# Kernel tuning notes

Measured on AMD Instinct MI355X. Metric: run time of the kernel, lower is better.

The kernel has to match this reference:

```python
import jax, jax.numpy as jnp
import numpy as np

B, N, D, NE, NB = 512, 128, 64, 6, 4

def setup_inputs() -> dict:
    key = jax.random.key(0)
    ks = jax.random.split(key, 24)
    inp = {}
    inp['atom_types'] = jax.random.randint(ks[0], (B, N), 0, NE, dtype=jnp.int32)
    inp['positions'] = jax.random.normal(ks[1], (B, N, 3), dtype=jnp.float32)
    inp['bonds'] = jax.random.randint(ks[2], (B, N, N), 0, 5, dtype=jnp.int32)
    s = 0.05
    inp['emb'] = jax.random.normal(ks[3], (NE, D), dtype=jnp.float32)
    inp['ae_w'] = jax.random.normal(ks[4], (D,), dtype=jnp.float32) * s
    inp['ae_b'] = jax.random.normal(ks[5], (), dtype=jnp.float32) * s
    inp['ent_w'] = jax.random.normal(ks[6], (D,), dtype=jnp.float32) * s
    inp['ent_b'] = jax.random.normal(ks[7], (), dtype=jnp.float32) * s
    inp['bW'] = jax.random.normal(ks[8], (NB, D, D), dtype=jnp.float32) * s
    inp['bb'] = jax.random.normal(ks[9], (NB,), dtype=jnp.float32) * s
    H = N * D
    inp['sW1'] = jax.random.normal(ks[10], (H, 256), dtype=jnp.float32) * s
    inp['sb1'] = jnp.zeros((256,), jnp.float32)
    inp['sW2'] = jax.random.normal(ks[11], (256, 128), dtype=jnp.float32) * s
    inp['sb2'] = jnp.zeros((128,), jnp.float32)
    inp['sW3'] = jax.random.normal(ks[12], (128, 1), dtype=jnp.float32) * s
    inp['sb3'] = jnp.zeros((1,), jnp.float32)
    inp['dW1'] = jax.random.normal(ks[13], (H, 256), dtype=jnp.float32) * s
    inp['db1'] = jnp.zeros((256,), jnp.float32)
    inp['dW2'] = jax.random.normal(ks[14], (256, 128), dtype=jnp.float32) * s
    inp['db2'] = jnp.zeros((128,), jnp.float32)
    inp['dW3'] = jax.random.normal(ks[15], (128, 1), dtype=jnp.float32) * s
    inp['db3'] = jnp.zeros((1,), jnp.float32)
    return inp

def _mlp(x, W1, b1, W2, b2, W3, b3):
    h = jax.nn.relu(x @ W1 + b1)
    h = jax.nn.relu(h @ W2 + b2)
    return jax.nn.sigmoid((h @ W3 + b3)[..., 0])

def reference(atom_types, positions, bonds, emb, ae_w, ae_b, ent_w, ent_b, bW, bb,
              sW1, sb1, sW2, sb2, sW3, sb3, dW1, db1, dW2, db2, dW3, db3):
    x = emb[atom_types]                                    # [B,N,D]
    atomic_e = jnp.einsum('bnd,d->bn', x, ae_w) + ae_b     # atomic_energy linear
    atomic_s = jnp.einsum('bnd,d->bn', x, ent_w) + ent_b   # atomic_entropy linear

    # Pairwise bilinear bond energies: e[b,i,j,k] = x_i^T W_k x_j + bb_k
    t = jnp.einsum('bid,kde->bike', x, bW)                 # [B,N,K,D]
    e_all = jnp.einsum('bike,bje->bijk', t, x) + bb        # [B,N,N,K]
    bt = bonds - 1                                         # bond type index
    upper = jnp.triu(jnp.ones((N, N), dtype=bool), k=1)    # i < j
    bond_mask = upper[None] & (bonds > 0) & (bt < NB)
    e_sel = jnp.take_along_axis(e_all, jnp.clip(bt, 0, NB - 1)[..., None].astype(jnp.int32), axis=-1)[..., 0]
    bond_e = jnp.sum(jnp.where(bond_mask, e_sel, 0.0), axis=(1, 2))

    # Lennard-Jones style vdW over all i<j pairs
    diff = positions[:, :, None, :] - positions[:, None, :, :]   # [B,N,N,3]
    dist = jnp.sqrt(jnp.sum(diff * diff, axis=-1))
    vmask = upper[None] & (dist > 0)
    inv = 1.0 / jnp.where(dist > 0, dist, 1.0)
    vdw = 4.0 * (inv ** 12 - inv ** 6) * 0.1
    vdw_e = jnp.sum(jnp.where(vmask, vdw, 0.0), axis=(1, 2))

    energy = atomic_e.sum(axis=1) + bond_e + vdw_e

    # entropy: unbiased variance over atoms, summed over xyz
    pos_var = jnp.var(positions, axis=1, ddof=1).sum(axis=-1)
    entropy = atomic_s.sum(axis=1) + jnp.log(1.0 + pos_var)

    mol = x.reshape(x.shape[0], -1)                        # [B, N*D]
    stability = _mlp(mol, sW1, sb1, sW2, sb2, sW3, sb3)
    druglikeness = _mlp(mol, dW1, db1, dW2, db2, dW3, db3)
    return (energy, entropy, stability, druglikeness, x)
```

## Files before the change

### kernel.cpp

```cpp
#include <hip/hip_runtime.h>
#include <math.h>

#define BB_ 512
#define NN_ 128
#define DD_ 64
#define NE_ 6
#define NB_ 4

#define WS_PAIRE 0
#define WS_AE    144
#define WS_ENT   152
#define WS_TS    160
#define WS_TD    (160 + 128 * 6 * 256)

__device__ __forceinline__ float block_reduce256(float v, volatile float* red4,
                                                 int tid) {
#pragma unroll
  for (int off = 32; off > 0; off >>= 1) v += __shfl_down(v, off);
  __syncthreads();
  if ((tid & 63) == 0) red4[tid >> 6] = v;
  __syncthreads();
  return red4[0] + red4[1] + red4[2] + red4[3];
}

__global__ __launch_bounds__(256, 4) void k_pre(
    const float* __restrict__ emb, const float* __restrict__ ae_w,
    const float* __restrict__ ae_b, const float* __restrict__ ent_w,
    const float* __restrict__ ent_b, const float* __restrict__ bW,
    const float* __restrict__ sW1, const float* __restrict__ dW1,
    float* __restrict__ ws, float* __restrict__ out) {
  int blk = blockIdx.x;
  int tid = threadIdx.x;

  if (blk < 512) {
    int n = blk >> 2;
    int which = (blk >> 1) & 1;
    int ohalf = blk & 1;
    const float* W1 = which ? dW1 : sW1;
    float* T = ws + (which ? WS_TD : WS_TS);
    __shared__ float e_s[NE_ * DD_];
    __shared__ float part[NE_][128];
    for (int i = tid; i < NE_ * DD_; i += 256) e_s[i] = emb[i];
    __syncthreads();
    int o_local = tid & 127;
    int dhalf = tid >> 7;
    int o = ohalf * 128 + o_local;
    float acc[NE_] = {0.f, 0.f, 0.f, 0.f, 0.f, 0.f};
    const float* Wp = W1 + ((size_t)(n * DD_ + dhalf * 32)) * 256 + o;
#pragma unroll 8
    for (int d = 0; d < 32; ++d) {
      float w = Wp[(size_t)d * 256];
#pragma unroll
      for (int t = 0; t < NE_; ++t) acc[t] += e_s[t * DD_ + dhalf * 32 + d] * w;
    }
    if (dhalf == 1) {
#pragma unroll
      for (int t = 0; t < NE_; ++t) part[t][o_local] = acc[t];
    }
    __syncthreads();
    if (dhalf == 0) {
#pragma unroll
      for (int t = 0; t < NE_; ++t)
        T[(n * NE_ + t) * 256 + o] = acc[t] + part[t][o_local];
    }
  } else if (blk == 512) {
    float4 z = make_float4(0.f, 0.f, 0.f, 0.f);
    ((float4*)out)[tid] = z;
  } else if (blk < 657) {
    int e = blk - 513;
    int k = e / 36;
    int rem = e - k * 36;
    int ti = rem / 6, tj = rem - (rem / 6) * 6;
    int d = tid & 63;
    int qd = tid >> 6;
    const float* Wrow = bW + ((size_t)k * DD_ + d) * DD_ + qd * 16;
    const float* xj = emb + tj * DD_ + qd * 16;
    float a = 0.f;
#pragma unroll
    for (int u = 0; u < 16; ++u) a += Wrow[u] * xj[u];
    float c = emb[ti * DD_ + d] * a;
    __shared__ float red4[4];
    c = block_reduce256(c, red4, tid);
    if (tid == 0) ws[WS_PAIRE + e] = c;
  } else {
    int g = tid >> 6, lane = tid & 63;
    for (int idx = g; idx < 12; idx += 4) {
      int t = idx - (idx >= 6 ? 6 : 0);
      bool ent = idx >= 6;
      float c = emb[t * DD_ + lane] * (ent ? ent_w[lane] : ae_w[lane]);
#pragma unroll
      for (int off = 32; off > 0; off >>= 1) c += __shfl_down(c, off);
      if (lane == 0)
        ws[(ent ? WS_ENT : WS_AE) + t] = c + (ent ? ent_b[0] : ae_b[0]);
    }
  }
}

__global__ __launch_bounds__(256, 4) void k_main(
    const int* __restrict__ atom_types, const float* __restrict__ pos,
    const int* __restrict__ bonds, const float* __restrict__ emb,
    const float* __restrict__ bb, const float* __restrict__ sb1,
    const float* __restrict__ sW2, const float* __restrict__ sb2,
    const float* __restrict__ sW3, const float* __restrict__ sb3,
    const float* __restrict__ db1, const float* __restrict__ dW2,
    const float* __restrict__ db2, const float* __restrict__ dW3,
    const float* __restrict__ db3, const float* __restrict__ ws,
    float* __restrict__ out) {
  int id = blockIdx.x;
  int tid = threadIdx.x;
  __shared__ float smem[3344];
  volatile float* red4 = smem + 3336;

  if (id < 128) {
    int which = id & 1;
    int mbase = (id >> 1) * 8;
    unsigned char* tyb = (unsigned char*)smem;
    float* h1 = smem + 256;
    float* h2 = smem + 2304;

    for (int u = tid; u < 8 * NN_; u += 256)
      tyb[u] = (unsigned char)atom_types[(size_t)mbase * NN_ + u];
    __syncthreads();

    {
      int mi = tid >> 5;
      int ot = tid & 31;
      const float* Tbase = ws + (which ? WS_TD : WS_TS) + ot * 8;
      const unsigned char* ty = tyb + mi * NN_;
      float4 a0 = make_float4(0.f, 0.f, 0.f, 0.f);
      float4 a1 = a0;
      for (int n0 = 0; n0 < NN_; n0 += 8) {
        float4 v0[8], v1[8];
#pragma unroll
        for (int u = 0; u < 8; ++u) {
          const float* row = Tbase + (((n0 + u) * 6 + (int)ty[n0 + u]) << 8);
          v0[u] = *(const float4*)row;
          v1[u] = *(const float4*)(row + 4);
        }
#pragma unroll
        for (int u = 0; u < 8; ++u) {
          a0.x += v0[u].x; a0.y += v0[u].y; a0.z += v0[u].z; a0.w += v0[u].w;
          a1.x += v1[u].x; a1.y += v1[u].y; a1.z += v1[u].z; a1.w += v1[u].w;
        }
      }
      const float* b1 = (which ? db1 : sb1) + ot * 8;
      float4 bb0 = *(const float4*)b1;
      float4 bb1 = *(const float4*)(b1 + 4);
      float* hp = h1 + mi * 256 + ot * 8;
      hp[0] = fmaxf(a0.x + bb0.x, 0.f);
      hp[1] = fmaxf(a0.y + bb0.y, 0.f);
      hp[2] = fmaxf(a0.z + bb0.z, 0.f);
      hp[3] = fmaxf(a0.w + bb0.w, 0.f);
      hp[4] = fmaxf(a1.x + bb1.x, 0.f);
      hp[5] = fmaxf(a1.y + bb1.y, 0.f);
      hp[6] = fmaxf(a1.z + bb1.z, 0.f);
      hp[7] = fmaxf(a1.w + bb1.w, 0.f);
    }
    __syncthreads();

    {
      int k = tid & 127;
      int kh = tid >> 7;
      const float* W2p =
          (which ? dW2 : sW2) + (size_t)(kh * 128) * 128 + k;
      float acc[8] = {0.f, 0.f, 0.f, 0.f, 0.f, 0.f, 0.f, 0.f};
      for (int o0 = 0; o0 < 128; o0 += 16) {
        float w[16];
#pragma unroll
        for (int u = 0; u < 16; ++u) w[u] = W2p[(size_t)(o0 + u) << 7];
#pragma unroll
        for (int mm = 0; mm < 8; ++mm) {
          const float4* hq = (const float4*)(h1 + mm * 256 + kh * 128 + o0);
          float4 q0 = hq[0], q1 = hq[1], q2 = hq[2], q3 = hq[3];
          acc[mm] += q0.x * w[0] + q0.y * w[1] + q0.z * w[2] + q0.w * w[3] +
                     q1.x * w[4] + q1.y * w[5] + q1.z * w[6] + q1.w * w[7] +
                     q2.x * w[8] + q2.y * w[9] + q2.z * w[10] + q2.w * w[11] +
                     q3.x * w[12] + q3.y * w[13] + q3.z * w[14] + q3.w * w[15];
        }
      }
      __syncthreads();
      float* scr = h1;
#pragma unroll
      for (int mm = 0; mm < 8; ++mm) scr[kh * 1024 + mm * 128 + k] = acc[mm];
      __syncthreads();
      if (tid < 128) {
        float b2v = (which ? db2 : sb2)[tid];
#pragma unroll
        for (int mm = 0; mm < 8; ++mm)
          h2[mm * 128 + tid] = fmaxf(
              b2v + scr[mm * 128 + tid] + scr[1024 + mm * 128 + tid], 0.f);
      }
      __syncthreads();
    }

    {
      int mm = tid >> 5;
      int ln = tid & 31;
      const float* W3 = which ? dW3 : sW3;
      float s = 0.f;
#pragma unroll
      for (int u = 0; u < 4; ++u) {
        int kk = ln + (u << 5);
        s += h2[mm * 128 + kk] * W3[kk];
      }
#pragma unroll
      for (int off = 16; off > 0; off >>= 1) s += __shfl_down(s, off, 32);
      if (ln == 0) {
        float b3 = (which ? db3 : sb3)[0];
        out[(2 + which) * BB_ + mbase + mm] = 1.f / (1.f + __expf(-(s + b3)));
      }
    }
  } else if (id < 640) {
    int m = id - 128;
    float* pE = smem;
    float* bbv = smem + 144;
    unsigned char* tyb = (unsigned char*)(smem + 160);

    if (tid < 32) {
      int4 t4 = ((const int4*)(atom_types + (size_t)m * NN_))[tid];
      uchar4 u4;
      u4.x = (unsigned char)t4.x;
      u4.y = (unsigned char)t4.y;
      u4.z = (unsigned char)t4.z;
      u4.w = (unsigned char)t4.w;
      ((uchar4*)tyb)[tid] = u4;
    }
    if (tid >= 64 && tid < 208) pE[tid - 64] = ws[WS_PAIRE + tid - 64];
    if (tid >= 224 && tid < 228) bbv[tid - 224] = bb[tid - 224];
    __syncthreads();

    const int4* b4 = (const int4*)(bonds + (size_t)m * NN_ * NN_);
    float bp = 0.f;
#pragma unroll 4
    for (int it = 0; it < 16; ++it) {
      int li = tid + (it << 8);
      int i = li >> 5;
      int c = li & 31;
      if (c * 4 + 3 > i) {
        int4 v = b4[li];
        int j0 = c << 2;
        int ti6 = tyb[i] * 6;
        if (j0 + 0 > i && v.x > 0)
          bp += pE[(v.x - 1) * 36 + ti6 + tyb[j0 + 0]] + bbv[v.x - 1];
        if (j0 + 1 > i && v.y > 0)
          bp += pE[(v.y - 1) * 36 + ti6 + tyb[j0 + 1]] + bbv[v.y - 1];
        if (j0 + 2 > i && v.z > 0)
          bp += pE[(v.z - 1) * 36 + ti6 + tyb[j0 + 2]] + bbv[v.z - 1];
        if (j0 + 3 > i && v.w > 0)
          bp += pE[(v.w - 1) * 36 + ti6 + tyb[j0 + 3]] + bbv[v.w - 1];
      }
    }
    float e = block_reduce256(bp, red4, tid);
    if (tid == 0) atomicAdd(&out[m], e);
  } else if (id < 1152) {
    int m = id - 640;
    float4* p4 = (float4*)smem;
    float* aev = smem + 520;
    float* entv = smem + 528;
    if (tid < 128) {
      const float* pm = pos + (size_t)m * NN_ * 3 + 3 * tid;
      p4[tid] = make_float4(pm[0], pm[1], pm[2], 0.f);
    }
    if (tid >= 128 && tid < 128 + NE_) aev[tid - 128] = ws[WS_AE + tid - 128];
    if (tid >= 160 && tid < 160 + NE_) entv[tid - 160] = ws[WS_ENT + tid - 160];
    __syncthreads();

    int i = tid >> 1;
    int half = tid & 1;
    float4 pi = p4[i];
    float vp = 0.f;
#pragma unroll 8
    for (int u = 0; u < 64; ++u) {
      int j = (half << 6) + u;
      float4 pj = p4[j];
      float dx = pi.x - pj.x;
      float dy = pi.y - pj.y;
      float dz = pi.z - pj.z;
      float d2 = dx * dx + dy * dy + dz * dz;
      if (j > i && d2 > 0.f) {
        float rc = __builtin_amdgcn_rcpf(d2);
        float r6 = rc * rc * rc;
        vp += 0.4f * (r6 * r6 - r6);
      }
    }

    float x = 0.f, y = 0.f, z = 0.f, sq = 0.f, ae = 0.f, en = 0.f;
    if (tid < 128) {
      float4 p = p4[tid];
      x = p.x;
      y = p.y;
      z = p.z;
      sq = x * x + y * y + z * z;
      int t = atom_types[(size_t)m * NN_ + tid];
      ae = aev[t];
      en = entv[t];
    }
    float Sv = block_reduce256(vp, red4, tid);
    float Sx = block_reduce256(x, red4, tid);
    float Sy = block_reduce256(y, red4, tid);
    float Sz = block_reduce256(z, red4, tid);
    float Ssq = block_reduce256(sq, red4, tid);
    float Sae = block_reduce256(ae, red4, tid);
    float Sen = block_reduce256(en, red4, tid);
    if (tid == 0) {
      float var = (Ssq - (Sx * Sx + Sy * Sy + Sz * Sz) * (1.f / NN_)) *
                  (1.f / (NN_ - 1));
      atomicAdd(&out[m], Sv + Sae);
      out[BB_ + m] = Sen + logf(1.f + var);
    }
  } else {
    int m = id - 1152;
    float* e_s = smem;
    unsigned char* tyb = (unsigned char*)(smem + 384);
    for (int i = tid; i < NE_ * DD_; i += 256) e_s[i] = emb[i];
    if (tid < 32) {
      int4 t4 = ((const int4*)(atom_types + (size_t)m * NN_))[tid];
      uchar4 u4;
      u4.x = (unsigned char)t4.x;
      u4.y = (unsigned char)t4.y;
      u4.z = (unsigned char)t4.z;
      u4.w = (unsigned char)t4.w;
      ((uchar4*)tyb)[tid] = u4;
    }
    __syncthreads();
    float4* out4 = (float4*)(out + 2048 + (size_t)m * (NN_ * DD_));
#pragma unroll
    for (int u = 0; u < 8; ++u) {
      int li = tid + (u << 8);
      int n = li >> 4;
      int d0 = (li & 15) << 2;
      out4[li] = *(const float4*)&e_s[tyb[n] * DD_ + d0];
    }
  }
}

extern "C" void kernel_launch(void* const* d_in, const int* in_sizes, int n_in,
                              void* d_out, int out_size, void* d_ws,
                              size_t ws_size, hipStream_t stream) {
  const int* atom_types = (const int*)d_in[0];
  const float* positions = (const float*)d_in[1];
  const int* bonds = (const int*)d_in[2];
  const float* emb = (const float*)d_in[3];
  const float* ae_w = (const float*)d_in[4];
  const float* ae_b = (const float*)d_in[5];
  const float* ent_w = (const float*)d_in[6];
  const float* ent_b = (const float*)d_in[7];
  const float* bW = (const float*)d_in[8];
  const float* bb = (const float*)d_in[9];
  const float* sW1 = (const float*)d_in[10];
  const float* sb1 = (const float*)d_in[11];
  const float* sW2 = (const float*)d_in[12];
  const float* sb2 = (const float*)d_in[13];
  const float* sW3 = (const float*)d_in[14];
  const float* sb3 = (const float*)d_in[15];
  const float* dW1 = (const float*)d_in[16];
  const float* db1 = (const float*)d_in[17];
  const float* dW2 = (const float*)d_in[18];
  const float* db2 = (const float*)d_in[19];
  const float* dW3 = (const float*)d_in[20];
  const float* db3 = (const float*)d_in[21];
  float* out = (float*)d_out;
  float* ws = (float*)d_ws;

  hipLaunchKernelGGL(k_pre, dim3(658), dim3(256), 0, stream, emb, ae_w, ae_b,
                     ent_w, ent_b, bW, sW1, dW1, ws, out);
  hipLaunchKernelGGL(k_main, dim3(1664), dim3(256), 0, stream, atom_types,
                     positions, bonds, emb, bb, sb1, sW2, sb2, sW3, sb3, db1,
                     dW2, db2, dW3, db3, ws, out);
}
```

Before: 34.48 us.

## Split MLP first-layer gather across per-molecule blocks and add tail kernel

Moves the embedding-output write into the pre-kernel. The MLP layer-1 gather, previously done by 128 blocks of 8 molecules each, is now spread across 1024 per-molecule blocks inside the main kernel, and h1 is written to workspace. A new third kernel runs layers 2 and 3 on 128 blocks. The bond path now prefetches all its bond loads into registers before the reduction. This spreads the serial gather over more CUs and interleaves block types per molecule, at the cost of an extra launch, a workspace round-trip for h1, and higher register pressure.

```diff
diff --git a/kernel.cpp b/kernel.cpp
--- a/kernel.cpp
+++ b/kernel.cpp
@@ -12,6 +12,7 @@
 #define WS_ENT   152
 #define WS_TS    160
 #define WS_TD    (160 + 128 * 6 * 256)
+#define WS_H1    (160 + 2 * 128 * 6 * 256)
 
 __device__ __forceinline__ float block_reduce256(float v, volatile float* red4,
                                                  int tid) {
@@ -28,7 +29,8 @@
     const float* __restrict__ ae_b, const float* __restrict__ ent_w,
     const float* __restrict__ ent_b, const float* __restrict__ bW,
     const float* __restrict__ sW1, const float* __restrict__ dW1,
-    float* __restrict__ ws, float* __restrict__ out) {
+    const int* __restrict__ atom_types, float* __restrict__ ws,
+    float* __restrict__ out) {
   int blk = blockIdx.x;
   int tid = threadIdx.x;
 
@@ -63,11 +65,34 @@
       for (int t = 0; t < NE_; ++t)
         T[(n * NE_ + t) * 256 + o] = acc[t] + part[t][o_local];
     }
-  } else if (blk == 512) {
+  } else if (blk < 1024) {
+    int m = blk - 512;
+    __shared__ float e_s[NE_ * DD_];
+    __shared__ unsigned char tyb[NN_];
+    for (int i = tid; i < NE_ * DD_; i += 256) e_s[i] = emb[i];
+    if (tid < 32) {
+      int4 t4 = ((const int4*)(atom_types + (size_t)m * NN_))[tid];
+      uchar4 u4;
+      u4.x = (unsigned char)t4.x;
+      u4.y = (unsigned char)t4.y;
+      u4.z = (unsigned char)t4.z;
+      u4.w = (unsigned char)t4.w;
+      ((uchar4*)tyb)[tid] = u4;
+    }
+    __syncthreads();
+    float4* out4 = (float4*)(out + 2048 + (size_t)m * (NN_ * DD_));
+#pragma unroll
+    for (int u = 0; u < 8; ++u) {
+      int li = tid + (u << 8);
+      int n = li >> 4;
+      int d0 = (li & 15) << 2;
+      out4[li] = *(const float4*)&e_s[tyb[n] * DD_ + d0];
+    }
+  } else if (blk == 1024) {
     float4 z = make_float4(0.f, 0.f, 0.f, 0.f);
     ((float4*)out)[tid] = z;
-  } else if (blk < 657) {
-    int e = blk - 513;
+  } else if (blk < 1169) {
+    int e = blk - 1025;
     int k = e / 36;
     int rem = e - k * 36;
     int ti = rem / 6, tj = rem - (rem / 6) * 6;
@@ -98,124 +123,33 @@
 
 __global__ __launch_bounds__(256, 4) void k_main(
     const int* __restrict__ atom_types, const float* __restrict__ pos,
-    const int* __restrict__ bonds, const float* __restrict__ emb,
-    const float* __restrict__ bb, const float* __restrict__ sb1,
-    const float* __restrict__ sW2, const float* __restrict__ sb2,
-    const float* __restrict__ sW3, const float* __restrict__ sb3,
-    const float* __restrict__ db1, const float* __restrict__ dW2,
-    const float* __restrict__ db2, const float* __restrict__ dW3,
-    const float* __restrict__ db3, const float* __restrict__ ws,
-    float* __restrict__ out) {
+    const int* __restrict__ bonds, const float* __restrict__ bb,
+    const float* __restrict__ sb1, const float* __restrict__ db1,
+    const float* __restrict__ ws, float* __restrict__ out,
+    float* __restrict__ wsmut) {
   int id = blockIdx.x;
+  int c = id & 3;
+  int m = id >> 2;
   int tid = threadIdx.x;
-  __shared__ float smem[3344];
-  volatile float* red4 = smem + 3336;
-
-  if (id < 128) {
-    int which = id & 1;
-    int mbase = (id >> 1) * 8;
-    unsigned char* tyb = (unsigned char*)smem;
-    float* h1 = smem + 256;
-    float* h2 = smem + 2304;
-
-    for (int u = tid; u < 8 * NN_; u += 256)
-      tyb[u] = (unsigned char)atom_types[(size_t)mbase * NN_ + u];
-    __syncthreads();
-
-    {
-      int mi = tid >> 5;
-      int ot = tid & 31;
-      const float* Tbase = ws + (which ? WS_TD : WS_TS) + ot * 8;
-      const unsigned char* ty = tyb + mi * NN_;
-      float4 a0 = make_float4(0.f, 0.f, 0.f, 0.f);
-      float4 a1 = a0;
-      for (int n0 = 0; n0 < NN_; n0 += 8) {
-        float4 v0[8], v1[8];
-#pragma unroll
-        for (int u = 0; u < 8; ++u) {
-          const float* row = Tbase + (((n0 + u) * 6 + (int)ty[n0 + u]) << 8);
-          v0[u] = *(const float4*)row;
-          v1[u] = *(const float4*)(row + 4);
-        }
-#pragma unroll
-        for (int u = 0; u < 8; ++u) {
-          a0.x += v0[u].x; a0.y += v0[u].y; a0.z += v0[u].z; a0.w += v0[u].w;
-          a1.x += v1[u].x; a1.y += v1[u].y; a1.z += v1[u].z; a1.w += v1[u].w;
-        }
-      }
-      const float* b1 = (which ? db1 : sb1) + ot * 8;
-      float4 bb0 = *(const float4*)b1;
-      float4 bb1 = *(const float4*)(b1 + 4);
-      float* hp = h1 + mi * 256 + ot * 8;
-      hp[0] = fmaxf(a0.x + bb0.x, 0.f);
-      hp[1] = fmaxf(a0.y + bb0.y, 0.f);
-      hp[2] = fmaxf(a0.z + bb0.z, 0.f);
-      hp[3] = fmaxf(a0.w + bb0.w, 0.f);
-      hp[4] = fmaxf(a1.x + bb1.x, 0.f);
-      hp[5] = fmaxf(a1.y + bb1.y, 0.f);
-      hp[6] = fmaxf(a1.z + bb1.z, 0.f);
-      hp[7] = fmaxf(a1.w + bb1.w, 0.f);
-    }
-    __syncthreads();
-
-    {
-      int k = tid & 127;
-      int kh = tid >> 7;
-      const float* W2p =
-          (which ? dW2 : sW2) + (size_t)(kh * 128) * 128 + k;
-      float acc[8] = {0.f, 0.f, 0.f, 0.f, 0.f, 0.f, 0.f, 0.f};
-      for (int o0 = 0; o0 < 128; o0 += 16) {
-        float w[16];
-#pragma unroll
-        for (int u = 0; u < 16; ++u) w[u] = W2p[(size_t)(o0 + u) << 7];
-#pragma unroll
-        for (int mm = 0; mm < 8; ++mm) {
-          const float4* hq = (const float4*)(h1 + mm * 256 + kh * 128 + o0);
-          float4 q0 = hq[0], q1 = hq[1], q2 = hq[2], q3 = hq[3];
-          acc[mm] += q0.x * w[0] + q0.y * w[1] + q0.z * w[2] + q0.w * w[3] +
-                     q1.x * w[4] + q1.y * w[5] + q1.z * w[6] + q1.w * w[7] +
-                     q2.x * w[8] + q2.y * w[9] + q2.z * w[10] + q2.w * w[11] +
-                     q3.x * w[12] + q3.y * w[13] + q3.z * w[14] + q3.w * w[15];
-        }
-      }
-      __syncthreads();
-      float* scr = h1;
-#pragma unroll
-      for (int mm = 0; mm < 8; ++mm) scr[kh * 1024 + mm * 128 + k] = acc[mm];
-      __syncthreads();
-      if (tid < 128) {
-        float b2v = (which ? db2 : sb2)[tid];
-#pragma unroll
-        for (int mm = 0; mm < 8; ++mm)
-          h2[mm * 128 + tid] = fmaxf(
-              b2v + scr[mm * 128 + tid] + scr[1024 + mm * 128 + tid], 0.f);
-      }
-      __syncthreads();
-    }
-
-    {
-      int mm = tid >> 5;
-      int ln = tid & 31;
-      const float* W3 = which ? dW3 : sW3;
-      float s = 0.f;
-#pragma unroll
-      for (int u = 0; u < 4; ++u) {
-        int kk = ln + (u << 5);
-        s += h2[mm * 128 + kk] * W3[kk];
-      }
-#pragma unroll
-      for (int off = 16; off > 0; off >>= 1) s += __shfl_down(s, off, 32);
-      if (ln == 0) {
-        float b3 = (which ? db3 : sb3)[0];
-        out[(2 + which) * BB_ + mbase + mm] = 1.f / (1.f + __expf(-(s + b3)));
-      }
-    }
-  } else if (id < 640) {
-    int m = id - 128;
+  __shared__ float smem[2064];
+  volatile float* red4 = smem + 2056;
+
+  if (c == 0) {
     float* pE = smem;
     float* bbv = smem + 144;
     unsigned char* tyb = (unsigned char*)(smem + 160);
 
+    const int4* b4 = (const int4*)(bonds + (size_t)m * NN_ * NN_);
+    int4 bv[16];
+    bool hv[16];
+#pragma unroll
+    for (int it = 0; it < 16; ++it) {
+      int li = tid + (it << 8);
+      int i = li >> 5;
+      int cc = li & 31;
+      hv[it] = (cc * 4 + 3 > i);
+      if (hv[it]) bv[it] = b4[li];
+    }
     if (tid < 32) {
       int4 t4 = ((const int4*)(atom_types + (size_t)m * NN_))[tid];
       uchar4 u4;
@@ -229,16 +163,14 @@
     if (tid >= 224 && tid < 228) bbv[tid - 224] = bb[tid - 224];
     __syncthreads();
 
-    const int4* b4 = (const int4*)(bonds + (size_t)m * NN_ * NN_);
     float bp = 0.f;
-#pragma unroll 4
+#pragma unroll
     for (int it = 0; it < 16; ++it) {
-      int li = tid + (it << 8);
-      int i = li >> 5;
-      int c = li & 31;
-      if (c * 4 + 3 > i) {
-        int4 v = b4[li];
-        int j0 = c << 2;
+      if (hv[it]) {
+        int li = tid + (it << 8);
+        int i = li >> 5;
+        int j0 = (li & 31) << 2;
+        int4 v = bv[it];
         int ti6 = tyb[i] * 6;
         if (j0 + 0 > i && v.x > 0)
           bp += pE[(v.x - 1) * 36 + ti6 + tyb[j0 + 0]] + bbv[v.x - 1];
@@ -252,8 +184,7 @@
     }
     float e = block_reduce256(bp, red4, tid);
     if (tid == 0) atomicAdd(&out[m], e);
-  } else if (id < 1152) {
-    int m = id - 640;
+  } else if (c == 1) {
     float4* p4 = (float4*)smem;
     float* aev = smem + 520;
     float* entv = smem + 528;
@@ -309,10 +240,9 @@
       out[BB_ + m] = Sen + logf(1.f + var);
     }
   } else {
-    int m = id - 1152;
-    float* e_s = smem;
-    unsigned char* tyb = (unsigned char*)(smem + 384);
-    for (int i = tid; i < NE_ * DD_; i += 256) e_s[i] = emb[i];
+    int which = id & 1;
+    unsigned char* tyb = (unsigned char*)(smem + 2048 - 32);
+    float* part = smem;
     if (tid < 32) {
       int4 t4 = ((const int4*)(atom_types + (size_t)m * NN_))[tid];
       uchar4 u4;
@@ -323,13 +253,126 @@
       ((uchar4*)tyb)[tid] = u4;
     }
     __syncthreads();
-    float4* out4 = (float4*)(out + 2048 + (size_t)m * (NN_ * DD_));
-#pragma unroll
-    for (int u = 0; u < 8; ++u) {
-      int li = tid + (u << 8);
-      int n = li >> 4;
-      int d0 = (li & 15) << 2;
-      out4[li] = *(const float4*)&e_s[tyb[n] * DD_ + d0];
+
+    int og = tid & 31;
+    int g = tid >> 5;
+    const float* Tbase = ws + (which ? WS_TD : WS_TS) + og * 8;
+    float4 a0 = make_float4(0.f, 0.f, 0.f, 0.f);
+    float4 a1 = a0;
+    {
+      int n0 = g * 16;
+      float4 v0[8], v1[8];
+#pragma unroll
+      for (int u = 0; u < 8; ++u) {
+        const float* row = Tbase + (((n0 + u) * 6 + (int)tyb[n0 + u]) << 8);
+        v0[u] = *(const float4*)row;
+        v1[u] = *(const float4*)(row + 4);
+      }
+      float4 w0[8], w1[8];
+#pragma unroll
+      for (int u = 0; u < 8; ++u) {
+        const float* row =
+            Tbase + (((n0 + 8 + u) * 6 + (int)tyb[n0 + 8 + u]) << 8);
+        w0[u] = *(const float4*)row;
+        w1[u] = *(const float4*)(row + 4);
+      }
+#pragma unroll
+      for (int u = 0; u < 8; ++u) {
+        a0.x += v0[u].x + w0[u].x;
+        a0.y += v0[u].y + w0[u].y;
+        a0.z += v0[u].z + w0[u].z;
+        a0.w += v0[u].w + w0[u].w;
+        a1.x += v1[u].x + w1[u].x;
+        a1.y += v1[u].y + w1[u].y;
+        a1.z += v1[u].z + w1[u].z;
+        a1.w += v1[u].w + w1[u].w;
+      }
+    }
+    __syncthreads();
+    float* pp = part + g * 256 + og * 8;
+    pp[0] = a0.x; pp[1] = a0.y; pp[2] = a0.z; pp[3] = a0.w;
+    pp[4] = a1.x; pp[5] = a1.y; pp[6] = a1.z; pp[7] = a1.w;
+    __syncthreads();
+    {
+      float s = 0.f;
+#pragma unroll
+      for (int gg = 0; gg < 8; ++gg) s += part[gg * 256 + tid];
+      float b1v = (which ? db1 : sb1)[tid];
+      wsmut[WS_H1 + ((size_t)(m * 2 + which) << 8) + tid] =
+          fmaxf(s + b1v, 0.f);
+    }
+  }
+}
+
+__global__ __launch_bounds__(256, 4) void k_tail(
+    const float* __restrict__ sW2, const float* __restrict__ sb2,
+    const float* __restrict__ sW3, const float* __restrict__ sb3,
+    const float* __restrict__ dW2, const float* __restrict__ db2,
+    const float* __restrict__ dW3, const float* __restrict__ db3,
+    const float* __restrict__ ws, float* __restrict__ out) {
+  int id = blockIdx.x;
+  int which = id & 1;
+  int g = id >> 1;
+  int tid = threadIdx.x;
+  __shared__ float h1s[2048];
+  __shared__ float h2[1024];
+
+  for (int li = tid; li < 2048; li += 256) {
+    int mm = li >> 8;
+    int o = li & 255;
+    h1s[li] = ws[WS_H1 + ((size_t)((g * 8 + mm) * 2 + which) << 8) + o];
+  }
+  __syncthreads();
+
+  {
+    int k = tid & 127;
+    int kh = tid >> 7;
+    const float* W2p = (which ? dW2 : sW2) + (size_t)(kh * 128) * 128 + k;
+    float acc[8] = {0.f, 0.f, 0.f, 0.f, 0.f, 0.f, 0.f, 0.f};
+    for (int o0 = 0; o0 < 128; o0 += 16) {
+      float w[16];
+#pragma unroll
+      for (int u = 0; u < 16; ++u) w[u] = W2p[(size_t)(o0 + u) << 7];
+#pragma unroll
+      for (int mm = 0; mm < 8; ++mm) {
+        const float4* hq = (const float4*)(h1s + mm * 256 + kh * 128 + o0);
+        float4 q0 = hq[0], q1 = hq[1], q2 = hq[2], q3 = hq[3];
+        acc[mm] += q0.x * w[0] + q0.y * w[1] + q0.z * w[2] + q0.w * w[3] +
+                   q1.x * w[4] + q1.y * w[5] + q1.z * w[6] + q1.w * w[7] +
+                   q2.x * w[8] + q2.y * w[9] + q2.z * w[10] + q2.w * w[11] +
+                   q3.x * w[12] + q3.y * w[13] + q3.z * w[14] + q3.w * w[15];
+      }
+    }
+    __syncthreads();
+    float* scr = h1s;
+#pragma unroll
+    for (int mm = 0; mm < 8; ++mm) scr[kh * 1024 + mm * 128 + k] = acc[mm];
+    __syncthreads();
+    if (tid < 128) {
+      float b2v = (which ? db2 : sb2)[tid];
+#pragma unroll
+      for (int mm = 0; mm < 8; ++mm)
+        h2[mm * 128 + tid] =
+            fmaxf(b2v + scr[mm * 128 + tid] + scr[1024 + mm * 128 + tid], 0.f);
+    }
+    __syncthreads();
+  }
+
+  {
+    int mm = tid >> 5;
+    int ln = tid & 31;
+    const float* W3 = which ? dW3 : sW3;
+    float s = 0.f;
+#pragma unroll
+    for (int u = 0; u < 4; ++u) {
+      int kk = ln + (u << 5);
+      s += h2[mm * 128 + kk] * W3[kk];
+    }
+#pragma unroll
+    for (int off = 16; off > 0; off >>= 1) s += __shfl_down(s, off, 32);
+    if (ln == 0) {
+      float b3 = (which ? db3 : sb3)[0];
+      out[(2 + which) * BB_ + g * 8 + mm] = 1.f / (1.f + __expf(-(s + b3)));
     }
   }
 }
@@ -362,9 +405,10 @@
   float* out = (float*)d_out;
   float* ws = (float*)d_ws;
 
-  hipLaunchKernelGGL(k_pre, dim3(658), dim3(256), 0, stream, emb, ae_w, ae_b,
-                     ent_w, ent_b, bW, sW1, dW1, ws, out);
-  hipLaunchKernelGGL(k_main, dim3(1664), dim3(256), 0, stream, atom_types,
-                     positions, bonds, emb, bb, sb1, sW2, sb2, sW3, sb3, db1,
-                     dW2, db2, dW3, db3, ws, out);
+  hipLaunchKernelGGL(k_pre, dim3(1170), dim3(256), 0, stream, emb, ae_w, ae_b,
+                     ent_w, ent_b, bW, sW1, dW1, atom_types, ws, out);
+  hipLaunchKernelGGL(k_main, dim3(2048), dim3(256), 0, stream, atom_types,
+                     positions, bonds, bb, sb1, db1, ws, out, ws);
+  hipLaunchKernelGGL(k_tail, dim3(128), dim3(256), 0, stream, sW2, sb2, sW3,
+                     sb3, dW2, db2, dW3, db3, ws, out);
 }
```

Result: slower. 47.23 us (+37.0%).

## Store MLP lookup tables and W2 in bf16, split MLP blocks finer

Applied to the files above, without the earlier changes.

The precomputed per-atom-type W1 projection tables and the W2 weights are converted to bf16 in the prep kernel, so the MLP gather reads half as many bytes. The MLP stage now handles 4 molecules per block instead of 8, doubling the block count, and splits the atom sum across two thread halves. The seven serial block reductions in the vdW/entropy block are merged into a single fused reduction with one sync. The cost is bf16 rounding of the weights, which may affect accuracy, plus an extra pass in the prep kernel.

```diff
diff --git a/kernel.cpp b/kernel.cpp
--- a/kernel.cpp
+++ b/kernel.cpp
@@ -10,8 +10,20 @@
 #define WS_PAIRE 0
 #define WS_AE    144
 #define WS_ENT   152
-#define WS_TS    160
-#define WS_TD    (160 + 128 * 6 * 256)
+#define U16BASE_ 256
+#define TDOFF_   (768 * 256)
+#define W2OFF_   (1536 * 256)
+
+typedef unsigned short u16x8 __attribute__((ext_vector_type(8)));
+
+__device__ __forceinline__ ushort f2b(float f) {
+  unsigned u = __float_as_uint(f);
+  u += 0x7FFFu + ((u >> 16) & 1u);
+  return (ushort)(u >> 16);
+}
+__device__ __forceinline__ float b2f(ushort h) {
+  return __uint_as_float(((unsigned)h) << 16);
+}
 
 __device__ __forceinline__ float block_reduce256(float v, volatile float* red4,
                                                  int tid) {
@@ -28,16 +40,18 @@
     const float* __restrict__ ae_b, const float* __restrict__ ent_w,
     const float* __restrict__ ent_b, const float* __restrict__ bW,
     const float* __restrict__ sW1, const float* __restrict__ dW1,
+    const float* __restrict__ sW2, const float* __restrict__ dW2,
     float* __restrict__ ws, float* __restrict__ out) {
   int blk = blockIdx.x;
   int tid = threadIdx.x;
+  ushort* U = (ushort*)(ws + U16BASE_);
 
   if (blk < 512) {
     int n = blk >> 2;
     int which = (blk >> 1) & 1;
     int ohalf = blk & 1;
     const float* W1 = which ? dW1 : sW1;
-    float* T = ws + (which ? WS_TD : WS_TS);
+    ushort* T = U + (which ? TDOFF_ : 0);
     __shared__ float e_s[NE_ * DD_];
     __shared__ float part[NE_][128];
     for (int i = tid; i < NE_ * DD_; i += 256) e_s[i] = emb[i];
@@ -61,7 +75,7 @@
     if (dhalf == 0) {
 #pragma unroll
       for (int t = 0; t < NE_; ++t)
-        T[(n * NE_ + t) * 256 + o] = acc[t] + part[t][o_local];
+        T[(n * NE_ + t) * 256 + o] = f2b(acc[t] + part[t][o_local]);
     }
   } else if (blk == 512) {
     float4 z = make_float4(0.f, 0.f, 0.f, 0.f);
@@ -82,7 +96,7 @@
     __shared__ float red4[4];
     c = block_reduce256(c, red4, tid);
     if (tid == 0) ws[WS_PAIRE + e] = c;
-  } else {
+  } else if (blk == 657) {
     int g = tid >> 6, lane = tid & 63;
     for (int idx = g; idx < 12; idx += 4) {
       int t = idx - (idx >= 6 ? 6 : 0);
@@ -93,6 +107,16 @@
       if (lane == 0)
         ws[(ent ? WS_ENT : WS_AE) + t] = c + (ent ? ent_b[0] : ae_b[0]);
     }
+  } else {
+    int base = (blk - 658) * 4096 + tid;
+#pragma unroll
+    for (int u = 0; u < 16; ++u) {
+      int e = base + u * 256;
+      int head = e >> 15;
+      int idx = e & 32767;
+      const float* src = head ? dW2 : sW2;
+      U[W2OFF_ + e] = f2b(src[idx]);
+    }
   }
 }
 
@@ -100,95 +124,92 @@
     const int* __restrict__ atom_types, const float* __restrict__ pos,
     const int* __restrict__ bonds, const float* __restrict__ emb,
     const float* __restrict__ bb, const float* __restrict__ sb1,
-    const float* __restrict__ sW2, const float* __restrict__ sb2,
-    const float* __restrict__ sW3, const float* __restrict__ sb3,
-    const float* __restrict__ db1, const float* __restrict__ dW2,
+    const float* __restrict__ sb2, const float* __restrict__ sW3,
+    const float* __restrict__ sb3, const float* __restrict__ db1,
     const float* __restrict__ db2, const float* __restrict__ dW3,
     const float* __restrict__ db3, const float* __restrict__ ws,
     float* __restrict__ out) {
   int id = blockIdx.x;
   int tid = threadIdx.x;
-  __shared__ float smem[3344];
-  volatile float* red4 = smem + 3336;
-
-  if (id < 128) {
+  const ushort* U = (const ushort*)(ws + U16BASE_);
+  __shared__ float smem[3216];
+  volatile float* red4 = smem + 3208;
+
+  if (id < 256) {
     int which = id & 1;
-    int mbase = (id >> 1) * 8;
-    unsigned char* tyb = (unsigned char*)smem;
-    float* h1 = smem + 256;
-    float* h2 = smem + 2304;
-
-    for (int u = tid; u < 8 * NN_; u += 256)
+    int mbase = (id >> 1) * 4;
+    unsigned char* tyb = (unsigned char*)(smem + 3072);
+    float* part = smem;
+    float* h1 = smem + 2048;
+    float* h2 = smem + 1024;
+
+    for (int u = tid; u < 4 * NN_; u += 256)
       tyb[u] = (unsigned char)atom_types[(size_t)mbase * NN_ + u];
     __syncthreads();
 
     {
-      int mi = tid >> 5;
+      int mi = tid >> 6;
+      int half = (tid >> 5) & 1;
       int ot = tid & 31;
-      const float* Tbase = ws + (which ? WS_TD : WS_TS) + ot * 8;
-      const unsigned char* ty = tyb + mi * NN_;
-      float4 a0 = make_float4(0.f, 0.f, 0.f, 0.f);
-      float4 a1 = a0;
-      for (int n0 = 0; n0 < NN_; n0 += 8) {
-        float4 v0[8], v1[8];
+      const ushort* Tb = U + (which ? TDOFF_ : 0) + ot * 8;
+      const unsigned char* ty = tyb + mi * NN_ + half * 64;
+      float a[8] = {0.f, 0.f, 0.f, 0.f, 0.f, 0.f, 0.f, 0.f};
+      for (int n0 = 0; n0 < 64; n0 += 8) {
+        u16x8 v[8];
 #pragma unroll
         for (int u = 0; u < 8; ++u) {
-          const float* row = Tbase + (((n0 + u) * 6 + (int)ty[n0 + u]) << 8);
-          v0[u] = *(const float4*)row;
-          v1[u] = *(const float4*)(row + 4);
+          int n = half * 64 + n0 + u;
+          v[u] = *(const u16x8*)(Tb + (((n * 6) + (int)ty[n0 + u]) << 8));
         }
 #pragma unroll
         for (int u = 0; u < 8; ++u) {
-          a0.x += v0[u].x; a0.y += v0[u].y; a0.z += v0[u].z; a0.w += v0[u].w;
-          a1.x += v1[u].x; a1.y += v1[u].y; a1.z += v1[u].z; a1.w += v1[u].w;
+#pragma unroll
+          for (int j = 0; j < 8; ++j) a[j] += b2f(v[u][j]);
         }
       }
-      const float* b1 = (which ? db1 : sb1) + ot * 8;
-      float4 bb0 = *(const float4*)b1;
-      float4 bb1 = *(const float4*)(b1 + 4);
-      float* hp = h1 + mi * 256 + ot * 8;
-      hp[0] = fmaxf(a0.x + bb0.x, 0.f);
-      hp[1] = fmaxf(a0.y + bb0.y, 0.f);
-      hp[2] = fmaxf(a0.z + bb0.z, 0.f);
-      hp[3] = fmaxf(a0.w + bb0.w, 0.f);
-      hp[4] = fmaxf(a1.x + bb1.x, 0.f);
-      hp[5] = fmaxf(a1.y + bb1.y, 0.f);
-      hp[6] = fmaxf(a1.z + bb1.z, 0.f);
-      hp[7] = fmaxf(a1.w + bb1.w, 0.f);
+      float* pp = part + mi * 512 + half * 256 + ot * 8;
+#pragma unroll
+      for (int j = 0; j < 8; ++j) pp[j] = a[j];
+    }
+    __syncthreads();
+    {
+      float b1v = (which ? db1 : sb1)[tid];
+#pragma unroll
+      for (int mm = 0; mm < 4; ++mm)
+        h1[mm * 256 + tid] =
+            fmaxf(part[mm * 512 + tid] + part[mm * 512 + 256 + tid] + b1v, 0.f);
     }
     __syncthreads();
 
     {
       int k = tid & 127;
       int kh = tid >> 7;
-      const float* W2p =
-          (which ? dW2 : sW2) + (size_t)(kh * 128) * 128 + k;
-      float acc[8] = {0.f, 0.f, 0.f, 0.f, 0.f, 0.f, 0.f, 0.f};
+      const ushort* Wp = U + W2OFF_ + which * 32768 + kh * 128 * 128 + k;
+      float acc[4] = {0.f, 0.f, 0.f, 0.f};
       for (int o0 = 0; o0 < 128; o0 += 16) {
-        float w[16];
-#pragma unroll
-        for (int u = 0; u < 16; ++u) w[u] = W2p[(size_t)(o0 + u) << 7];
-#pragma unroll
-        for (int mm = 0; mm < 8; ++mm) {
-          const float4* hq = (const float4*)(h1 + mm * 256 + kh * 128 + o0);
-          float4 q0 = hq[0], q1 = hq[1], q2 = hq[2], q3 = hq[3];
-          acc[mm] += q0.x * w[0] + q0.y * w[1] + q0.z * w[2] + q0.w * w[3] +
-                     q1.x * w[4] + q1.y * w[5] + q1.z * w[6] + q1.w * w[7] +
-                     q2.x * w[8] + q2.y * w[9] + q2.z * w[10] + q2.w * w[11] +
-                     q3.x * w[12] + q3.y * w[13] + q3.z * w[14] + q3.w * w[15];
+        float wf[16];
+#pragma unroll
+        for (int u = 0; u < 16; ++u) wf[u] = b2f(Wp[(o0 + u) << 7]);
+#pragma unroll
+        for (int mm = 0; mm < 4; ++mm) {
+          const float* hp = h1 + mm * 256 + kh * 128 + o0;
+          float s = 0.f;
+#pragma unroll
+          for (int u = 0; u < 16; ++u) s += hp[u] * wf[u];
+          acc[mm] += s;
         }
       }
       __syncthreads();
-      float* scr = h1;
-#pragma unroll
-      for (int mm = 0; mm < 8; ++mm) scr[kh * 1024 + mm * 128 + k] = acc[mm];
+      float* scr = part;
+#pragma unroll
+      for (int mm = 0; mm < 4; ++mm) scr[kh * 512 + mm * 128 + k] = acc[mm];
       __syncthreads();
       if (tid < 128) {
         float b2v = (which ? db2 : sb2)[tid];
 #pragma unroll
-        for (int mm = 0; mm < 8; ++mm)
+        for (int mm = 0; mm < 4; ++mm)
           h2[mm * 128 + tid] = fmaxf(
-              b2v + scr[mm * 128 + tid] + scr[1024 + mm * 128 + tid], 0.f);
+              b2v + scr[mm * 128 + tid] + scr[512 + mm * 128 + tid], 0.f);
       }
       __syncthreads();
     }
@@ -196,22 +217,24 @@
     {
       int mm = tid >> 5;
       int ln = tid & 31;
-      const float* W3 = which ? dW3 : sW3;
-      float s = 0.f;
-#pragma unroll
-      for (int u = 0; u < 4; ++u) {
-        int kk = ln + (u << 5);
-        s += h2[mm * 128 + kk] * W3[kk];
-      }
-#pragma unroll
-      for (int off = 16; off > 0; off >>= 1) s += __shfl_down(s, off, 32);
-      if (ln == 0) {
-        float b3 = (which ? db3 : sb3)[0];
-        out[(2 + which) * BB_ + mbase + mm] = 1.f / (1.f + __expf(-(s + b3)));
-      }
-    }
-  } else if (id < 640) {
-    int m = id - 128;
+      if (mm < 4) {
+        const float* W3 = which ? dW3 : sW3;
+        float s = 0.f;
+#pragma unroll
+        for (int u = 0; u < 4; ++u) {
+          int kk = ln + (u << 5);
+          s += h2[mm * 128 + kk] * W3[kk];
+        }
+#pragma unroll
+        for (int off = 16; off > 0; off >>= 1) s += __shfl_down(s, off, 32);
+        if (ln == 0) {
+          float b3 = (which ? db3 : sb3)[0];
+          out[(2 + which) * BB_ + mbase + mm] = 1.f / (1.f + __expf(-(s + b3)));
+        }
+      }
+    }
+  } else if (id < 768) {
+    int m = id - 256;
     float* pE = smem;
     float* bbv = smem + 144;
     unsigned char* tyb = (unsigned char*)(smem + 160);
@@ -252,11 +275,12 @@
     }
     float e = block_reduce256(bp, red4, tid);
     if (tid == 0) atomicAdd(&out[m], e);
-  } else if (id < 1152) {
-    int m = id - 640;
+  } else if (id < 1280) {
+    int m = id - 768;
     float4* p4 = (float4*)smem;
     float* aev = smem + 520;
     float* entv = smem + 528;
+    float* redm = smem + 544;
     if (tid < 128) {
       const float* pm = pos + (size_t)m * NN_ * 3 + 3 * tid;
       p4[tid] = make_float4(pm[0], pm[1], pm[2], 0.f);
@@ -295,21 +319,32 @@
       ae = aev[t];
       en = entv[t];
     }
-    float Sv = block_reduce256(vp, red4, tid);
-    float Sx = block_reduce256(x, red4, tid);
-    float Sy = block_reduce256(y, red4, tid);
-    float Sz = block_reduce256(z, red4, tid);
-    float Ssq = block_reduce256(sq, red4, tid);
-    float Sae = block_reduce256(ae, red4, tid);
-    float Sen = block_reduce256(en, red4, tid);
+    float vals[7] = {vp, x, y, z, sq, ae, en};
+#pragma unroll
+    for (int v = 0; v < 7; ++v) {
+#pragma unroll
+      for (int off = 32; off > 0; off >>= 1)
+        vals[v] += __shfl_down(vals[v], off);
+    }
+    int wv = tid >> 6, ln = tid & 63;
+    if (ln == 0) {
+#pragma unroll
+      for (int v = 0; v < 7; ++v) redm[wv * 8 + v] = vals[v];
+    }
+    __syncthreads();
     if (tid == 0) {
-      float var = (Ssq - (Sx * Sx + Sy * Sy + Sz * Sz) * (1.f / NN_)) *
+      float S[7];
+#pragma unroll
+      for (int v = 0; v < 7; ++v)
+        S[v] = redm[v] + redm[8 + v] + redm[16 + v] + redm[24 + v];
+      float var = (S[4] - (S[1] * S[1] + S[2] * S[2] + S[3] * S[3]) *
+                              (1.f / NN_)) *
                   (1.f / (NN_ - 1));
-      atomicAdd(&out[m], Sv + Sae);
-      out[BB_ + m] = Sen + logf(1.f + var);
+      atomicAdd(&out[m], S[0] + S[5]);
+      out[BB_ + m] = S[6] + logf(1.f + var);
     }
   } else {
-    int m = id - 1152;
+    int m = id - 1280;
     float* e_s = smem;
     unsigned char* tyb = (unsigned char*)(smem + 384);
     for (int i = tid; i < NE_ * DD_; i += 256) e_s[i] = emb[i];
@@ -362,9 +397,9 @@
   float* out = (float*)d_out;
   float* ws = (float*)d_ws;
 
-  hipLaunchKernelGGL(k_pre, dim3(658), dim3(256), 0, stream, emb, ae_w, ae_b,
-                     ent_w, ent_b, bW, sW1, dW1, ws, out);
-  hipLaunchKernelGGL(k_main, dim3(1664), dim3(256), 0, stream, atom_types,
-                     positions, bonds, emb, bb, sb1, sW2, sb2, sW3, sb3, db1,
-                     dW2, db2, dW3, db3, ws, out);
-}
+  hipLaunchKernelGGL(k_pre, dim3(674), dim3(256), 0, stream, emb, ae_w, ae_b,
+                     ent_w, ent_b, bW, sW1, dW1, sW2, dW2, ws, out);
+  hipLaunchKernelGGL(k_main, dim3(1792), dim3(256), 0, stream, atom_types,
+                     positions, bonds, emb, bb, sb1, sb2, sW3, sb3, db1, db2,
+                     dW3, db3, ws, out);
+}
```

Result: faster. 27.85 us, median of 2 (-19.2%).
